# Optimization experiments

Hardware: AMD Instinct MI355X
Metric: run time of the kernel (lower is better)

The kernel has to match this reference:

```python
import jax, jax.numpy as jnp
import numpy as np

HIDDEN = 1024
RANK = 4
INPUT = 16
ALPHA = 0.1
BASE_SCALE = 500.0
B = 32
T = 1024


def setup_inputs() -> dict:
    key = jax.random.key(0)
    k1, k2, k3, k4 = jax.random.split(key, 4)
    std = HIDDEN ** -0.25  # matches cov ~ I/sqrt(hidden) in original init
    x = jax.random.normal(k1, (B, T, INPUT), dtype=jnp.float32)
    m = jax.random.normal(k2, (HIDDEN, RANK), dtype=jnp.float32) * std
    n = jax.random.normal(k3, (HIDDEN, RANK), dtype=jnp.float32) * std
    I_mat = jax.random.normal(k4, (HIDDEN, INPUT), dtype=jnp.float32) * std
    return {"x": x, "m": m, "n": n, "I_mat": I_mat}


def reference(x, m, n, I_mat):
    # J = (m @ n.T) * base_scale / hidden ; recurrent term (J @ tanh(h).T).T
    # == tanh(h) @ J.T == ((tanh(h) @ n) @ m.T) * scale  (low-rank form, same math)
    scale = BASE_SCALE / HIDDEN

    def step(h, x_t):
        rec = (jnp.tanh(h) @ n) @ m.T * scale          # [B, H]
        dh = -h + rec + x_t @ I_mat.T                  # [B, H]
        h = h + ALPHA * dh
        return h, h

    h0 = jnp.zeros((x.shape[0], HIDDEN), dtype=x.dtype)
    _, hiddens = jax.lax.scan(step, h0, jnp.swapaxes(x, 0, 1))  # [T, B, H]
    hiddens = jnp.swapaxes(hiddens, 0, 1)                       # [B, T, H]

    span = jnp.concatenate([m, I_mat], axis=1)   # [H, RANK+INPUT]
    proj = jnp.linalg.pinv(span)                 # [RANK+INPUT, H]
    # (pinv(span) @ hiddens.permute(0,2,1)).permute(0,2,1)
    return jnp.einsum('ph,bth->btp', proj, hiddens)  # [B, T, RANK+INPUT]
```

## Files before the change

kernel.cpp:

```cpp
#include <hip/hip_runtime.h>
#include <math.h>

#define HIDDEN_ 1024
#define RANK_ 4
#define INPUT_ 16
#define T_ 1024
#define BATCH_ 32

#define NT_ 512
#define SCANT_ 256
#define EPT_ 4
#define CH_ 64
#define NCH_ (T_ / CH_)

__device__ __forceinline__ float fast_exp2(float x) {
#if defined(__has_builtin)
#if __has_builtin(__builtin_amdgcn_exp2f)
    return __builtin_amdgcn_exp2f(x);
#else
    return exp2f(x);
#endif
#else
    return exp2f(x);
#endif
}

__device__ __forceinline__ float fast_rcp(float x) {
#if defined(__has_builtin)
#if __has_builtin(__builtin_amdgcn_rcpf)
    return __builtin_amdgcn_rcpf(x);
#else
    return 1.0f / x;
#endif
#else
    return 1.0f / x;
#endif
}

__device__ __forceinline__ float tanh_fast(float x) {
    float e = fast_exp2(x * 2.885390081777926815f);
    return fmaf(-2.0f, fast_rcp(e + 1.0f), 1.0f);
}

#define DPP_ADD(v, ctrl)                                                          \
    do {                                                                          \
        int _t = __builtin_amdgcn_update_dpp(0, __float_as_int(v), (ctrl), 0xf,   \
                                             0xf, true);                          \
        (v) += __int_as_float(_t);                                                \
    } while (0)

__global__ __launch_bounds__(NT_)
__attribute__((amdgpu_waves_per_eu(2, 2)))
void rnn_fused_kernel(
    const float* __restrict__ x,
    const float* __restrict__ m,
    const float* __restrict__ n,
    const float* __restrict__ imat,
    float* __restrict__ out)
{
    const int tid  = threadIdx.x;
    const int lane = tid & 63;
    const int b    = blockIdx.x;
    const bool is_scan = (tid < SCANT_);

    const float kd   = 0.9f;
    const float krec = 0.1f * (500.0f / 1024.0f);
    const float kin  = 0.1f;

    __shared__ float4 part[2][SCANT_ / 64];
    __shared__ float  axs[4][HIDDEN_];
    __shared__ float  xs[2][CH_ * INPUT_];

    const float* xb = x + (size_t)b * T_ * INPUT_;
    float* ob = out + (size_t)b * T_ * (RANK_ + INPUT_);

    float h[EPT_];
    float mrs[EPT_][RANK_];
    float nr[EPT_][RANK_];
    float Irs[EPT_][INPUT_];
    float4 xstage = make_float4(0.f, 0.f, 0.f, 0.f);
    float y = 0.0f;
    int yoff = 0;

    if (is_scan) {
#pragma unroll
        for (int j = 0; j < EPT_; ++j) {
            const int hidx = tid * EPT_ + j;
            h[j] = 0.0f;
            const float4 mv = *(const float4*)(m + hidx * RANK_);
            mrs[j][0] = krec * mv.x; mrs[j][1] = krec * mv.y;
            mrs[j][2] = krec * mv.z; mrs[j][3] = krec * mv.w;
            const float4 nv = *(const float4*)(n + hidx * RANK_);
            nr[j][0] = nv.x; nr[j][1] = nv.y; nr[j][2] = nv.z; nr[j][3] = nv.w;
        }
    } else {
        const int tH = tid - SCANT_;
        yoff = (tH >= 4 && tH < 20) ? (tH - 4) : 0;
#pragma unroll
        for (int j = 0; j < EPT_; ++j) {
            const int hidx = tH * EPT_ + j;
#pragma unroll
            for (int q = 0; q < 4; ++q) {
                const float4 iv = *(const float4*)(imat + hidx * INPUT_ + q * 4);
                Irs[j][q*4+0] = kin * iv.x; Irs[j][q*4+1] = kin * iv.y;
                Irs[j][q*4+2] = kin * iv.z; Irs[j][q*4+3] = kin * iv.w;
            }
        }
        float4 c0 = *(const float4*)(xb + tH * 4);
        *(float4*)&xs[0][tH * 4] = c0;
        xstage = *(const float4*)(xb + CH_ * INPUT_ + tH * 4);
        float xv[INPUT_];
#pragma unroll
        for (int q = 0; q < 4; ++q) {
            const float4 v = ((const float4*)xb)[q];
            xv[q*4+0] = v.x; xv[q*4+1] = v.y; xv[q*4+2] = v.z; xv[q*4+3] = v.w;
        }
        float av[EPT_];
#pragma unroll
        for (int j = 0; j < EPT_; ++j) {
            float a = xv[0] * Irs[j][0];
            float c = xv[1] * Irs[j][1];
#pragma unroll
            for (int i = 2; i < INPUT_; i += 2) {
                a = fmaf(xv[i],     Irs[j][i],     a);
                c = fmaf(xv[i + 1], Irs[j][i + 1], c);
            }
            av[j] = a + c;
        }
        *(float4*)&axs[0][tH * 4] = make_float4(av[0], av[1], av[2], av[3]);
    }
    __syncthreads();

    for (int t = 0; t < T_; ++t) {
        if (is_scan) {
            float th[EPT_];
#pragma unroll
            for (int j = 0; j < EPT_; ++j) th[j] = tanh_fast(h[j]);

            float p0 = th[0] * nr[0][0], p1 = th[0] * nr[0][1];
            float p2 = th[0] * nr[0][2], p3 = th[0] * nr[0][3];
#pragma unroll
            for (int j = 1; j < EPT_; ++j) {
                p0 = fmaf(th[j], nr[j][0], p0);
                p1 = fmaf(th[j], nr[j][1], p1);
                p2 = fmaf(th[j], nr[j][2], p2);
                p3 = fmaf(th[j], nr[j][3], p3);
            }

            DPP_ADD(p0, 0x111); DPP_ADD(p1, 0x111); DPP_ADD(p2, 0x111); DPP_ADD(p3, 0x111);
            DPP_ADD(p0, 0x112); DPP_ADD(p1, 0x112); DPP_ADD(p2, 0x112); DPP_ADD(p3, 0x112);
            DPP_ADD(p0, 0x114); DPP_ADD(p1, 0x114); DPP_ADD(p2, 0x114); DPP_ADD(p3, 0x114);
            DPP_ADD(p0, 0x118); DPP_ADD(p1, 0x118); DPP_ADD(p2, 0x118); DPP_ADD(p3, 0x118);
            DPP_ADD(p0, 0x142); DPP_ADD(p1, 0x142); DPP_ADD(p2, 0x142); DPP_ADD(p3, 0x142);
            DPP_ADD(p0, 0x143); DPP_ADD(p1, 0x143); DPP_ADD(p2, 0x143); DPP_ADD(p3, 0x143);

            if (lane == 63) part[t & 1][tid >> 6] = make_float4(p0, p1, p2, p3);
        } else {
            const int tH = tid - SCANT_;
            const int tn = (t + 1 < T_) ? (t + 1) : (T_ - 1);
            const float* xsp = &xs[(tn >> 6) & 1][(tn & 63) * INPUT_];
            const float4 xa  = ((const float4*)xsp)[0];
            const float4 xb4 = ((const float4*)xsp)[1];
            const float4 xc  = ((const float4*)xsp)[2];
            const float4 xd  = ((const float4*)xsp)[3];
            float av[EPT_];
#pragma unroll
            for (int j = 0; j < EPT_; ++j) {
                float a = xa.x * Irs[j][0];
                float c = xa.y * Irs[j][1];
                a = fmaf(xa.z,  Irs[j][2],  a);  c = fmaf(xa.w,  Irs[j][3],  c);
                a = fmaf(xb4.x, Irs[j][4],  a);  c = fmaf(xb4.y, Irs[j][5],  c);
                a = fmaf(xb4.z, Irs[j][6],  a);  c = fmaf(xb4.w, Irs[j][7],  c);
                a = fmaf(xc.x,  Irs[j][8],  a);  c = fmaf(xc.y,  Irs[j][9],  c);
                a = fmaf(xc.z,  Irs[j][10], a);  c = fmaf(xc.w,  Irs[j][11], c);
                a = fmaf(xd.x,  Irs[j][12], a);  c = fmaf(xd.y,  Irs[j][13], c);
                a = fmaf(xd.z,  Irs[j][14], a);  c = fmaf(xd.w,  Irs[j][15], c);
                av[j] = a + c;
            }
            *(float4*)&axs[(t + 1) & 3][tH * 4] =
                make_float4(av[0], av[1], av[2], av[3]);
        }

        asm volatile("s_waitcnt lgkmcnt(0)\n\ts_barrier" ::: "memory");

        if (is_scan) {
            const float4 q0 = part[t & 1][0];
            const float4 q1 = part[t & 1][1];
            const float4 q2 = part[t & 1][2];
            const float4 q3 = part[t & 1][3];
            const float4 axv = *(const float4*)&axs[t & 3][tid * 4];

            const float4 sv = (q0 + q1) + (q2 + q3);
            const float s0 = sv.x, s1 = sv.y, s2 = sv.z, s3 = sv.w;
            const float aq[EPT_] = {axv.x, axv.y, axv.z, axv.w};
#pragma unroll
            for (int j = 0; j < EPT_; ++j) {
                float a01 = fmaf(s1, mrs[j][1], fmaf(s0, mrs[j][0], aq[j]));
                float a23 = fmaf(s3, mrs[j][3], s2 * mrs[j][2]);
                h[j] = fmaf(kd, h[j], a01 + a23);
            }
        } else {
            const int tH = tid - SCANT_;
            if ((t & (CH_ - 1)) == 0) {
                const int c = t >> 6;
                *(float4*)&xs[(c + 1) & 1][tH * 4] = xstage;
                const int cl = (c + 2 < NCH_) ? (c + 2) : (NCH_ - 1);
                xstage = *(const float4*)(xb + cl * CH_ * INPUT_ + tH * 4);
            }
            if (tH < 20) {
                const float4 q0 = part[t & 1][0];
                const float4 q1 = part[t & 1][1];
                const float4 q2 = part[t & 1][2];
                const float4 q3 = part[t & 1][3];
                const float4 sv = (q0 + q1) + (q2 + q3);
                float drive;
                if (tH < 4) {
                    const float svv = (tH == 0) ? sv.x : (tH == 1) ? sv.y
                                    : (tH == 2) ? sv.z : sv.w;
                    drive = krec * svv;
                } else {
                    drive = kin * xs[(t >> 6) & 1][(t & 63) * INPUT_ + yoff];
                }
                y = fmaf(kd, y, drive);
                ob[t * 20 + tH] = y;
            }
        }
    }
}

extern "C" void kernel_launch(void* const* d_in, const int* in_sizes, int n_in,
                              void* d_out, int out_size, void* d_ws, size_t ws_size,
                              hipStream_t stream) {
    const float* x    = (const float*)d_in[0];
    const float* m    = (const float*)d_in[1];
    const float* n    = (const float*)d_in[2];
    const float* imat = (const float*)d_in[3];
    float* out = (float*)d_out;

    rnn_fused_kernel<<<dim3(BATCH_), dim3(NT_), 0, stream>>>(x, m, n, imat, out);
}
```

Before: 518.7 us.

## Split input projection into precompute kernel and run scan with one wave per batch

Adds a parallel kernel that writes the input drive x@I^T*0.1 for every (b,t) into a 128 MiB workspace. The recurrence then runs as a single 64-lane wave per batch, holding 16 hidden units per lane and reducing with DPP plus readlane, so no per-step block barrier or LDS exchange is needed. This removes per-timestep synchronisation latency. The cost is four times more serial work per lane, a large extra HBM write and read stream for u, and a dependence on having enough workspace; without it the old fused kernel is used.

```diff
diff --git a/kernel.cpp b/kernel.cpp
--- a/kernel.cpp
+++ b/kernel.cpp
@@ -6,6 +6,14 @@
 #define INPUT_ 16
 #define T_ 1024
 #define BATCH_ 32
+
+#define SW_ 64
+#define EPT1_ (HIDDEN_ / SW_)
+
+#define PRE_TPB_ 256
+#define PRE_BLOCKS_ 2048
+#define ROWS_ (BATCH_ * T_)
+#define PASSES_ (ROWS_ / PRE_BLOCKS_)
 
 #define NT_ 512
 #define SCANT_ 256
@@ -49,13 +57,196 @@
         (v) += __int_as_float(_t);                                                \
     } while (0)
 
+__device__ __forceinline__ float readlane63(float v) {
+    return __int_as_float(__builtin_amdgcn_readlane(__float_as_int(v), 63));
+}
+
+__global__ __launch_bounds__(PRE_TPB_, 2) void precompute_u(
+    const float* __restrict__ x,
+    const float* __restrict__ imat,
+    float* __restrict__ u)
+{
+    const int tid = threadIdx.x;
+    const int bid = blockIdx.x;
+    const float kin = 0.1f;
+
+    float Ir[4][INPUT_];
+#pragma unroll
+    for (int r = 0; r < 4; ++r) {
+        const float* ip = imat + (4 * tid + r) * INPUT_;
+#pragma unroll
+        for (int q = 0; q < 4; ++q) {
+            const float4 v = *(const float4*)(ip + 4 * q);
+            Ir[r][q*4+0] = kin * v.x; Ir[r][q*4+1] = kin * v.y;
+            Ir[r][q*4+2] = kin * v.z; Ir[r][q*4+3] = kin * v.w;
+        }
+    }
+
+    for (int p = 0; p < PASSES_; ++p) {
+        const int row = p * PRE_BLOCKS_ + bid;
+        const float* xr = x + (size_t)row * INPUT_;
+        float xv[INPUT_];
+#pragma unroll
+        for (int q = 0; q < 4; ++q) {
+            const float4 v = ((const float4*)xr)[q];
+            xv[q*4+0] = v.x; xv[q*4+1] = v.y; xv[q*4+2] = v.z; xv[q*4+3] = v.w;
+        }
+        float a[4];
+#pragma unroll
+        for (int r = 0; r < 4; ++r) {
+            float s0 = xv[0] * Ir[r][0];
+            float s1 = xv[1] * Ir[r][1];
+#pragma unroll
+            for (int i = 2; i < INPUT_; i += 2) {
+                s0 = fmaf(xv[i],     Ir[r][i],     s0);
+                s1 = fmaf(xv[i + 1], Ir[r][i + 1], s1);
+            }
+            a[r] = s0 + s1;
+        }
+        float4 acc = make_float4(a[0], a[1], a[2], a[3]);
+        *(float4*)(u + (size_t)row * HIDDEN_ + 4 * tid) = acc;
+    }
+}
+
+__global__ __launch_bounds__(SW_)
+__attribute__((amdgpu_waves_per_eu(1, 1)))
+void rnn_scan1w(
+    const float* __restrict__ x,
+    const float* __restrict__ m,
+    const float* __restrict__ n,
+    const float* __restrict__ u,
+    float* __restrict__ out)
+{
+    const int lane = threadIdx.x;
+    const int b    = blockIdx.x;
+
+    const float kd   = 0.9f;
+    const float krec = 0.1f * (500.0f / 1024.0f);
+    const float kin  = 0.1f;
+
+    float h[EPT1_];
+    float mrs[EPT1_][RANK_];
+    float nr[EPT1_][RANK_];
+#pragma unroll
+    for (int j = 0; j < EPT1_; ++j) {
+        const int hidx = lane * EPT1_ + j;
+        h[j] = 0.0f;
+        const float4 mv = *(const float4*)(m + hidx * RANK_);
+        mrs[j][0] = krec * mv.x; mrs[j][1] = krec * mv.y;
+        mrs[j][2] = krec * mv.z; mrs[j][3] = krec * mv.w;
+        const float4 nv = *(const float4*)(n + hidx * RANK_);
+        nr[j][0] = nv.x; nr[j][1] = nv.y; nr[j][2] = nv.z; nr[j][3] = nv.w;
+    }
+
+    const float* xb = x + (size_t)b * T_ * INPUT_;
+    const float* ub = u + (size_t)b * T_ * HIDDEN_ + lane * EPT1_;
+    float* ob = out + (size_t)b * T_ * (RANK_ + INPUT_);
+
+    const int xoff = (lane >= 4 && lane < 20) ? (lane - 4) : 0;
+
+    float4 upf[4][4];
+    float xpf[4];
+#pragma unroll
+    for (int k = 0; k < 4; ++k) {
+        const float* up = ub + (size_t)k * HIDDEN_;
+        upf[k][0] = *(const float4*)(up);
+        upf[k][1] = *(const float4*)(up + 4);
+        upf[k][2] = *(const float4*)(up + 8);
+        upf[k][3] = *(const float4*)(up + 12);
+        xpf[k] = xb[k * INPUT_ + xoff];
+    }
+
+    float y = 0.0f;
+
+#define SW_STEP(k)                                                               \
+    {                                                                            \
+        const int t = tb + (k);                                                  \
+                \
+        const float4 u0 = upf[k][0], u1 = upf[k][1];                             \
+        const float4 u2 = upf[k][2], u3 = upf[k][3];                             \
+        const float xcur = xpf[k];                                               \
+        {                                                                        \
+            int tn = t + 4; if (tn >= T_) tn = T_ - 1;                           \
+            const float* up = ub + (size_t)tn * HIDDEN_;                         \
+            upf[k][0] = *(const float4*)(up);                                    \
+            upf[k][1] = *(const float4*)(up + 4);                                \
+            upf[k][2] = *(const float4*)(up + 8);                                \
+            upf[k][3] = *(const float4*)(up + 12);                               \
+            xpf[k] = xb[tn * INPUT_ + xoff];                                     \
+        }                                                                        \
+                                                                       \
+        float th[EPT1_];                                                         \
+        _Pragma("unroll")                                                        \
+        for (int j = 0; j < EPT1_; ++j) th[j] = tanh_fast(h[j]);                 \
+                                           \
+        float p[RANK_], q[RANK_];                                                \
+        _Pragma("unroll")                                                        \
+        for (int r = 0; r < RANK_; ++r) {                                        \
+            p[r] = th[0] * nr[0][r];                                             \
+            q[r] = th[1] * nr[1][r];                                             \
+        }                                                                        \
+        _Pragma("unroll")                                                        \
+        for (int j = 2; j < EPT1_; j += 2) {                                     \
+            _Pragma("unroll")                                                    \
+            for (int r = 0; r < RANK_; ++r) {                                    \
+                p[r] = fmaf(th[j],     nr[j][r],     p[r]);                      \
+                q[r] = fmaf(th[j + 1], nr[j + 1][r], q[r]);                      \
+            }                                                                    \
+        }                                                                        \
+        _Pragma("unroll")                                                        \
+        for (int r = 0; r < RANK_; ++r) p[r] += q[r];                            \
+                                \
+        DPP_ADD(p[0], 0x111); DPP_ADD(p[1], 0x111); DPP_ADD(p[2], 0x111); DPP_ADD(p[3], 0x111); \
+        DPP_ADD(p[0], 0x112); DPP_ADD(p[1], 0x112); DPP_ADD(p[2], 0x112); DPP_ADD(p[3], 0x112); \
+        DPP_ADD(p[0], 0x114); DPP_ADD(p[1], 0x114); DPP_ADD(p[2], 0x114); DPP_ADD(p[3], 0x114); \
+        DPP_ADD(p[0], 0x118); DPP_ADD(p[1], 0x118); DPP_ADD(p[2], 0x118); DPP_ADD(p[3], 0x118); \
+        DPP_ADD(p[0], 0x142); DPP_ADD(p[1], 0x142); DPP_ADD(p[2], 0x142); DPP_ADD(p[3], 0x142); \
+        DPP_ADD(p[0], 0x143); DPP_ADD(p[1], 0x143); DPP_ADD(p[2], 0x143); DPP_ADD(p[3], 0x143); \
+                         \
+        const float s0 = readlane63(p[0]);                                       \
+        const float s1 = readlane63(p[1]);                                       \
+        const float s2 = readlane63(p[2]);                                       \
+        const float s3 = readlane63(p[3]);                                       \
+                                                      \
+        const float uq[EPT1_] = {u0.x, u0.y, u0.z, u0.w, u1.x, u1.y, u1.z, u1.w, \
+                                 u2.x, u2.y, u2.z, u2.w, u3.x, u3.y, u3.z, u3.w};\
+        _Pragma("unroll")                                                        \
+        for (int j = 0; j < EPT1_; ++j) {                                        \
+            float a = fmaf(s0, mrs[j][0], uq[j]);                                \
+            a = fmaf(s1, mrs[j][1], a);                                          \
+            a = fmaf(s2, mrs[j][2], a);                                          \
+            a = fmaf(s3, mrs[j][3], a);                                          \
+            h[j] = fmaf(kd, h[j], a);                                            \
+        }                                                                        \
+                                      \
+        if (lane < 20) {                                                         \
+            float drive;                                                         \
+            if (lane < 4) {                                                      \
+                const float sv = (lane == 0) ? s0 : (lane == 1) ? s1             \
+                               : (lane == 2) ? s2 : s3;                          \
+                drive = krec * sv;                                               \
+            } else {                                                             \
+                drive = kin * xcur;                                              \
+            }                                                                    \
+            y = fmaf(kd, y, drive);                                              \
+            ob[t * 20 + lane] = y;                                               \
+        }                                                                        \
+    }
+
+    for (int tb = 0; tb < T_; tb += 4) {
+        SW_STEP(0)
+        SW_STEP(1)
+        SW_STEP(2)
+        SW_STEP(3)
+    }
+#undef SW_STEP
+}
+
 __global__ __launch_bounds__(NT_)
 __attribute__((amdgpu_waves_per_eu(2, 2)))
 void rnn_fused_kernel(
-    const float* __restrict__ x,
-    const float* __restrict__ m,
-    const float* __restrict__ n,
-    const float* __restrict__ imat,
+    const float* __restrict__ x, const float* __restrict__ m,
+    const float* __restrict__ n, const float* __restrict__ imat,
     float* __restrict__ out)
 {
     const int tid  = threadIdx.x;
@@ -136,7 +327,6 @@
             float th[EPT_];
 #pragma unroll
             for (int j = 0; j < EPT_; ++j) th[j] = tanh_fast(h[j]);
-
             float p0 = th[0] * nr[0][0], p1 = th[0] * nr[0][1];
             float p2 = th[0] * nr[0][2], p3 = th[0] * nr[0][3];
 #pragma unroll
@@ -146,14 +336,12 @@
                 p2 = fmaf(th[j], nr[j][2], p2);
                 p3 = fmaf(th[j], nr[j][3], p3);
             }
-
             DPP_ADD(p0, 0x111); DPP_ADD(p1, 0x111); DPP_ADD(p2, 0x111); DPP_ADD(p3, 0x111);
             DPP_ADD(p0, 0x112); DPP_ADD(p1, 0x112); DPP_ADD(p2, 0x112); DPP_ADD(p3, 0x112);
             DPP_ADD(p0, 0x114); DPP_ADD(p1, 0x114); DPP_ADD(p2, 0x114); DPP_ADD(p3, 0x114);
             DPP_ADD(p0, 0x118); DPP_ADD(p1, 0x118); DPP_ADD(p2, 0x118); DPP_ADD(p3, 0x118);
             DPP_ADD(p0, 0x142); DPP_ADD(p1, 0x142); DPP_ADD(p2, 0x142); DPP_ADD(p3, 0x142);
             DPP_ADD(p0, 0x143); DPP_ADD(p1, 0x143); DPP_ADD(p2, 0x143); DPP_ADD(p3, 0x143);
-
             if (lane == 63) part[t & 1][tid >> 6] = make_float4(p0, p1, p2, p3);
         } else {
             const int tH = tid - SCANT_;
@@ -189,7 +377,6 @@
             const float4 q2 = part[t & 1][2];
             const float4 q3 = part[t & 1][3];
             const float4 axv = *(const float4*)&axs[t & 3][tid * 4];
-
             const float4 sv = (q0 + q1) + (q2 + q3);
             const float s0 = sv.x, s1 = sv.y, s2 = sv.z, s3 = sv.w;
             const float aq[EPT_] = {axv.x, axv.y, axv.z, axv.w};
@@ -237,5 +424,12 @@
     const float* imat = (const float*)d_in[3];
     float* out = (float*)d_out;
 
-    rnn_fused_kernel<<<dim3(BATCH_), dim3(NT_), 0, stream>>>(x, m, n, imat, out);
-}
+    const size_t u_bytes = (size_t)BATCH_ * T_ * HIDDEN_ * sizeof(float);
+    if (d_ws != nullptr && ws_size >= u_bytes) {
+        float* u = (float*)d_ws;
+        precompute_u<<<dim3(PRE_BLOCKS_), dim3(PRE_TPB_), 0, stream>>>(x, imat, u);
+        rnn_scan1w<<<dim3(BATCH_), dim3(SW_), 0, stream>>>(x, m, n, u, out);
+    } else {
+        rnn_fused_kernel<<<dim3(BATCH_), dim3(NT_), 0, stream>>>(x, m, n, imat, out);
+    }
+}
```

Measured after the change: 633.6 us. 22.2% more time.
